# Kernel optimization log

Hardware: AMD Instinct MI355X
Metric: run time of the kernel (lower is better)

## Reference

```python
import jax, jax.numpy as jnp
import numpy as np

B, C, H, W = 8, 256, 64, 64
IC = 64  # inter_channels


def conv1x1(x, w, b):
    # x: [B,C,H,W], w: [O,C], b: [O]
    return jnp.einsum('bchw,oc->bohw', x, w) + b[None, :, None, None]


def maxpool2(x):
    # 2x2 max pool, stride 2. x: [B,C,H,W]
    b, c, h, w = x.shape
    return x.reshape(b, c, h // 2, 2, w // 2, 2).max(axis=(3, 5))


def setup_inputs() -> dict:
    key = jax.random.key(0)
    ks = jax.random.split(key, 9)
    s_in = 1.0 / np.sqrt(C)
    s_ic = 1.0 / np.sqrt(IC)
    return {
        'x': jax.random.normal(ks[0], (B, C, H, W), dtype=jnp.float32),
        'g_w': jax.random.uniform(ks[1], (IC, C), jnp.float32, -s_in, s_in),
        'g_b': jax.random.uniform(ks[2], (IC,), jnp.float32, -s_in, s_in),
        'theta_w': jax.random.uniform(ks[3], (IC, C), jnp.float32, -s_in, s_in),
        'theta_b': jax.random.uniform(ks[4], (IC,), jnp.float32, -s_in, s_in),
        'phi_w': jax.random.uniform(ks[5], (IC, C), jnp.float32, -s_in, s_in),
        'phi_b': jax.random.uniform(ks[6], (IC,), jnp.float32, -s_in, s_in),
        'W_w': jax.random.uniform(ks[7], (C, IC), jnp.float32, -np.sqrt(6.0 / IC), np.sqrt(6.0 / IC)),
        'W_b': jax.random.uniform(ks[8], (C,), jnp.float32, -s_ic, s_ic),
    }


def reference(x, g_w, g_b, theta_w, theta_b, phi_w, phi_b, W_w, W_b):
    b, c, h, w = x.shape
    n = h * w                     # query positions
    m = (h // 2) * (w // 2)       # pooled key/value positions

    v = maxpool2(conv1x1(x, g_w, g_b)).reshape(b, IC, m).transpose(0, 2, 1)   # [b,m,ic]
    q = conv1x1(x, theta_w, theta_b).reshape(b, IC, n).transpose(0, 2, 1)     # [b,n,ic]
    k = maxpool2(conv1x1(x, phi_w, phi_b)).reshape(b, IC, m)                  # [b,ic,m]

    attn = jax.nn.softmax(jnp.einsum('bni,bim->bnm', q, k), axis=-1)          # [b,n,m]
    attended = jnp.einsum('bnm,bmi->bni', attn, v)                            # [b,n,ic]
    attended = attended.transpose(0, 2, 1).reshape(b, IC, h, w)
    # F.interpolate to (h,w) is identity here: attended already has spatial (h,w)
    return conv1x1(attended, W_w, W_b) + x
```

## Files before the change

kernel.cpp:

```cpp
#include <hip/hip_runtime.h>

typedef unsigned short ushort_t;
typedef unsigned int   uint_t;

typedef __attribute__((ext_vector_type(8))) short  short8;
typedef __attribute__((ext_vector_type(4))) short  short4v;
typedef __attribute__((ext_vector_type(4))) float  float4v;

#define BB    8
#define CC    256
#define HH    64
#define WW2   64
#define NPIX  4096
#define MPOS  1024
#define ICH   64

__device__ __forceinline__ float bf2f(ushort_t u) {
  return __uint_as_float(((uint_t)u) << 16);
}
__device__ __forceinline__ ushort_t f2bf(float f) {
  uint_t i = __float_as_uint(f);
  uint_t r = (i + 0x7FFFu + ((i >> 16) & 1u)) >> 16;
  return (ushort_t)r;
}
__device__ __forceinline__ ushort_t f2bf_rna(float f) {
  return (ushort_t)((__float_as_uint(f) + 0x8000u) >> 16);
}
__device__ __forceinline__ uint_t pack2(float a, float b) {
  return (uint_t)f2bf(a) | ((uint_t)f2bf(b) << 16);
}

__global__ __launch_bounds__(256) void prep_kernel(
    const float* __restrict__ theta_w, const float* __restrict__ phi_w,
    const float* __restrict__ g_w, const float* __restrict__ W_w,
    const float* __restrict__ theta_b, const float* __restrict__ phi_b,
    const float* __restrict__ g_b,
    ushort_t* __restrict__ wA2, ushort_t* __restrict__ Wbf2,
    float* __restrict__ biasAll) {
  int i = blockIdx.x * 256 + threadIdx.x;
  if (i < 49152) {
    float v = (i < 16384) ? theta_w[i]
            : (i < 32768) ? phi_w[i - 16384]
                          : g_w[i - 32768];
    int o = i >> 8, c = i & 255;
    wA2[(c >> 3) * 1536 + o * 8 + (c & 7)] = f2bf(v);
  } else if (i < 65536) {
    int j = i - 49152;
    int o = j >> 6, ic = j & 63;
    Wbf2[(ic >> 3) * 2048 + o * 8 + (ic & 7)] = f2bf(W_w[j]);
  } else if (i < 65600)    biasAll[i - 65536] = theta_b[i - 65536];
  else if (i < 65664)      biasAll[i - 65536] = phi_b[i - 65600];
  else if (i < 65728)      biasAll[i - 65536] = g_b[i - 65664];
}

__global__ __launch_bounds__(256, 2) void qkv_kernel(
    const float* __restrict__ x, const ushort_t* __restrict__ wA2,
    const float* __restrict__ biasAll,
    ushort_t* __restrict__ qbuf, ushort_t* __restrict__ kTbuf,
    ushort_t* __restrict__ vTbuf) {
  __shared__ __align__(16) ushort_t Bsu[64 * 256];
  uint4* Bs16 = (uint4*)Bsu;
  int tid = threadIdx.x;
  int wave = tid >> 6, lane = tid & 63;
  int quad = lane >> 4, col = lane & 15;
  int b = blockIdx.x >> 6, t = blockIdx.x & 63;
  int rj = t >> 1, h = t & 1;

  {
    int pos = tid & 63, cg = tid >> 6;
    int prow = pos >> 5, pcol = pos & 31;
    const float* xsrc = x + (size_t)b * (CC * NPIX) +
                        (size_t)(2 * rj + prow) * WW2 + h * 32 + pcol;
#pragma unroll
    for (int g = 0; g < 8; ++g) {
      float v[8];
#pragma unroll
      for (int j = 0; j < 8; ++j)
        v[j] = xsrc[(size_t)(cg * 64 + g * 8 + j) * NPIX];
      uint4 w;
      w.x = pack2(v[0], v[1]);
      w.y = pack2(v[2], v[3]);
      w.z = pack2(v[4], v[5]);
      w.w = pack2(v[6], v[7]);
      int jb = cg * 8 + g;
      Bs16[pos * 32 + (jb & ~7) + ((jb & 7) ^ (pos & 7))] = w;
    }
  }
  __syncthreads();

  float4v acc[3][4];
#pragma unroll
  for (int ot = 0; ot < 3; ++ot) {
    int ob = wave * 48 + ot * 16 + quad * 4;
    float4v bv;
#pragma unroll
    for (int r = 0; r < 4; ++r) bv[r] = biasAll[ob + r];
#pragma unroll
    for (int s = 0; s < 4; ++s) acc[ot][s] = bv;
  }

  const uint4* wA16 = (const uint4*)wA2;
#pragma unroll
  for (int ks = 0; ks < 8; ++ks) {
    int kblk = ks * 4 + quad;
    short8 aw[3];
#pragma unroll
    for (int ot = 0; ot < 3; ++ot) {
      uint4 a = wA16[kblk * 192 + wave * 48 + ot * 16 + col];
      aw[ot] = *(const short8*)&a;
    }
#pragma unroll
    for (int s = 0; s < 4; ++s) {
      int lp = s * 16 + col;
      uint4 braw = Bs16[lp * 32 + (kblk & ~7) + ((kblk & 7) ^ (lp & 7))];
      short8 bx = *(const short8*)&braw;
#pragma unroll
      for (int ot = 0; ot < 3; ++ot)
        acc[ot][s] = __builtin_amdgcn_mfma_f32_16x16x32_bf16(aw[ot], bx, acc[ot][s], 0, 0, 0);
    }
  }

#pragma unroll
  for (int ot = 0; ot < 3; ++ot) {
    int ob = wave * 48 + ot * 16;
    if (ob < 64) {
#pragma unroll
      for (int s = 0; s < 4; ++s) {
        int n = (2 * rj + (s >> 1)) * WW2 + h * 32 + (s & 1) * 16 + col;
        uint2 u;
        u.x = pack2(acc[ot][s][0], acc[ot][s][1]);
        u.y = pack2(acc[ot][s][2], acc[ot][s][3]);
        *(uint2*)&qbuf[((size_t)(b * NPIX + n)) * ICH + ob + quad * 4] = u;
      }
    } else if (ob < 128) {
#pragma unroll
      for (int s = 0; s < 2; ++s) {
        float4v pm;
#pragma unroll
        for (int r = 0; r < 4; ++r) {
          float v = fmaxf(acc[ot][s][r], acc[ot][s + 2][r]);
          pm[r] = fmaxf(v, __shfl_xor(v, 1));
        }
        if ((lane & 1) == 0) {
          int m = rj * 32 + h * 16 + s * 8 + (col >> 1);
          uint2 u;
          u.x = pack2(pm[0], pm[1]);
          u.y = pack2(pm[2], pm[3]);
          *(uint2*)&kTbuf[((size_t)(b * MPOS + m)) * ICH + (ob - 64) + quad * 4] = u;
        }
      }
    } else {
#pragma unroll
      for (int s = 0; s < 2; ++s) {
        float4v pm;
#pragma unroll
        for (int r = 0; r < 4; ++r) {
          float v = fmaxf(acc[ot][s][r], acc[ot][s + 2][r]);
          pm[r] = fmaxf(v, __shfl_xor(v, 1));
        }
        if ((lane & 1) == 0) {
          int m = rj * 32 + h * 16 + s * 8 + (col >> 1);
#pragma unroll
          for (int r = 0; r < 4; ++r)
            vTbuf[((size_t)(b * ICH + (ob - 128) + quad * 4 + r)) * MPOS + m] = f2bf(pm[r]);
        }
      }
    }
  }
}

__global__ __launch_bounds__(256, 2) void attn_out_kernel(
    const ushort_t* __restrict__ qbuf, const ushort_t* __restrict__ kTbuf,
    const ushort_t* __restrict__ vTbuf, const ushort_t* __restrict__ Wbf2,
    const float* __restrict__ W_b, const float* __restrict__ x,
    float* __restrict__ out) {
  __shared__ __align__(16) ushort_t Ks[2][64 * 64];
  __shared__ __align__(16) ushort_t Vs[2][64 * 64];
  __shared__ __align__(16) ushort_t Ps[64 * 72];
  int tid  = threadIdx.x;
  int wave = tid >> 6, lane = tid & 63;
  int quad = lane >> 4, col = lane & 15;
  int b = blockIdx.x >> 6, qt = blockIdx.x & 63;

  const ushort_t* qrow = qbuf + ((size_t)(b * NPIX + qt * 64 + wave * 16 + col)) * ICH;
  short8 aQ0 = *(const short8*)&qrow[quad * 8];
  short8 aQ1 = *(const short8*)&qrow[32 + quad * 8];

  int krow0 = tid >> 3,           kblk0 = tid & 7;
  int krow1 = (tid + 256) >> 3,   kblk1 = tid & 7;
  int vic = tid >> 2, vseg = tid & 3;

  const uint4* ksrc0 = (const uint4*)(kTbuf + ((size_t)(b * MPOS)) * ICH);
  const ushort_t* vbase = vTbuf + ((size_t)(b * ICH + vic)) * MPOS;

  {
    uint4 k0 = ksrc0[tid], k1 = ksrc0[tid + 256];
    const uint4* vsrc = (const uint4*)(vbase + vseg * 16);
    uint4 v0 = vsrc[0], v1 = vsrc[1];
    *(uint4*)&Ks[0][krow0 * 64 + ((kblk0 ^ (krow0 & 7)) * 8)] = k0;
    *(uint4*)&Ks[0][krow1 * 64 + ((kblk1 ^ (krow1 & 7)) * 8)] = k1;
    *(uint4*)&Vs[0][vic * 64 + (((vseg * 2 + 0) ^ (vic & 7)) * 8)] = v0;
    *(uint4*)&Vs[0][vic * 64 + (((vseg * 2 + 1) ^ (vic & 7)) * 8)] = v1;
  }
  __syncthreads();

  const float4v zero4 = {0.f, 0.f, 0.f, 0.f};
  float l_lane[4] = {0.f, 0.f, 0.f, 0.f};
  float4v o_acc[4];
#pragma unroll
  for (int t = 0; t < 4; ++t) o_acc[t] = zero4;

  for (int kt = 0; kt < 16; ++kt) {
    uint4 nk0, nk1, nv0, nv1;
    if (kt < 15) {
      const uint4* ksrc = (const uint4*)(kTbuf + ((size_t)(b * MPOS + (kt + 1) * 64)) * ICH);
      nk0 = ksrc[tid];
      nk1 = ksrc[tid + 256];
      const uint4* vsrc = (const uint4*)(vbase + (kt + 1) * 64 + vseg * 16);
      nv0 = vsrc[0];
      nv1 = vsrc[1];
    }
    int buf = kt & 1;

    float4v s_acc[4];
#pragma unroll
    for (int t = 0; t < 4; ++t) {
      float4v s = zero4;
      short8 bk0 = *(const short8*)&Ks[buf][(t * 16 + col) * 64 + ((quad ^ (col & 7)) * 8)];
      s = __builtin_amdgcn_mfma_f32_16x16x32_bf16(aQ0, bk0, s, 0, 0, 0);
      short8 bk1 = *(const short8*)&Ks[buf][(t * 16 + col) * 64 + (((4 + quad) ^ (col & 7)) * 8)];
      s = __builtin_amdgcn_mfma_f32_16x16x32_bf16(aQ1, bk1, s, 0, 0, 0);
      s_acc[t] = s;
    }

#pragma unroll
    for (int r = 0; r < 4; ++r) {
      int prow = (wave * 16 + quad * 4 + r) * 72;
#pragma unroll
      for (int t = 0; t < 4; ++t) {
        float pv = __expf(s_acc[t][r]);
        l_lane[r] += pv;
        Ps[prow + t * 16 + col] = f2bf_rna(pv);
      }
    }

#pragma unroll
    for (int kk = 0; kk < 2; ++kk) {
      short8 ap = *(const short8*)&Ps[(wave * 16 + col) * 72 + kk * 32 + quad * 8];
#pragma unroll
      for (int t = 0; t < 4; ++t) {
        short8 bv = *(const short8*)&Vs[buf][(t * 16 + col) * 64 + (((kk * 4 + quad) ^ (col & 7)) * 8)];
        o_acc[t] = __builtin_amdgcn_mfma_f32_16x16x32_bf16(ap, bv, o_acc[t], 0, 0, 0);
      }
    }

    if (kt < 15) {
      int nbuf = buf ^ 1;
      *(uint4*)&Ks[nbuf][krow0 * 64 + ((kblk0 ^ (krow0 & 7)) * 8)] = nk0;
      *(uint4*)&Ks[nbuf][krow1 * 64 + ((kblk1 ^ (krow1 & 7)) * 8)] = nk1;
      *(uint4*)&Vs[nbuf][vic * 64 + (((vseg * 2 + 0) ^ (vic & 7)) * 8)] = nv0;
      *(uint4*)&Vs[nbuf][vic * 64 + (((vseg * 2 + 1) ^ (vic & 7)) * 8)] = nv1;
      __syncthreads();
    }
  }

#pragma unroll
  for (int r = 0; r < 4; ++r) {
    float l = l_lane[r];
    l += __shfl_xor(l, 1);
    l += __shfl_xor(l, 2);
    l += __shfl_xor(l, 4);
    l += __shfl_xor(l, 8);
    float inv = 1.0f / l;
    int prow = (wave * 16 + quad * 4 + r) * 72;
#pragma unroll
    for (int t = 0; t < 4; ++t)
      Ps[prow + t * 16 + col] = f2bf(o_acc[t][r] * inv);
  }

  float4v cacc[16];
#pragma unroll
  for (int ot = 0; ot < 16; ++ot) {
    float bv = W_b[ot * 16 + col];
    float4v bvec = {bv, bv, bv, bv};
    cacc[ot] = bvec;
  }
  const uint4* W16 = (const uint4*)Wbf2;
#pragma unroll
  for (int ks = 0; ks < 2; ++ks) {
    short8 ap = *(const short8*)&Ps[(wave * 16 + col) * 72 + ks * 32 + quad * 8];
#pragma unroll
    for (int ot = 0; ot < 16; ++ot) {
      uint4 wr = W16[(ks * 4 + quad) * 256 + ot * 16 + col];
      short8 wf = *(const short8*)&wr;
      cacc[ot] = __builtin_amdgcn_mfma_f32_16x16x32_bf16(ap, wf, cacc[ot], 0, 0, 0);
    }
  }

  int pbase = qt * 64 + wave * 16 + quad * 4;
#pragma unroll
  for (int ot = 0; ot < 16; ++ot) {
    int o = ot * 16 + col;
    size_t idx = ((size_t)(b * CC + o)) * NPIX + pbase;
    float4 xv = *(const float4*)&x[idx];
    float4 ov;
    ov.x = cacc[ot][0] + xv.x;
    ov.y = cacc[ot][1] + xv.y;
    ov.z = cacc[ot][2] + xv.z;
    ov.w = cacc[ot][3] + xv.w;
    *(float4*)&out[idx] = ov;
  }
}

extern "C" void kernel_launch(void* const* d_in, const int* in_sizes, int n_in,
                              void* d_out, int out_size, void* d_ws, size_t ws_size,
                              hipStream_t stream) {
  const float* x       = (const float*)d_in[0];
  const float* g_w     = (const float*)d_in[1];
  const float* g_b     = (const float*)d_in[2];
  const float* theta_w = (const float*)d_in[3];
  const float* theta_b = (const float*)d_in[4];
  const float* phi_w   = (const float*)d_in[5];
  const float* phi_b   = (const float*)d_in[6];
  const float* W_w     = (const float*)d_in[7];
  const float* W_b     = (const float*)d_in[8];
  (void)in_sizes; (void)n_in; (void)out_size; (void)ws_size;

  char* ws = (char*)d_ws;
  ushort_t* wA2     = (ushort_t*)(ws + 0);
  ushort_t* Wbf2    = (ushort_t*)(ws + 98304);
  float*    biasAll = (float*)(ws + 131072);
  ushort_t* qbuf    = (ushort_t*)(ws + 262144);
  ushort_t* kTbuf   = (ushort_t*)(ws + 4456448);
  ushort_t* vTbuf   = (ushort_t*)(ws + 5505024);
  float* out = (float*)d_out;

  prep_kernel<<<257, 256, 0, stream>>>(theta_w, phi_w, g_w, W_w,
                                       theta_b, phi_b, g_b,
                                       wA2, Wbf2, biasAll);
  qkv_kernel<<<512, 256, 0, stream>>>(x, wA2, biasAll, qbuf, kTbuf, vTbuf);
  attn_out_kernel<<<512, 256, 0, stream>>>(qbuf, kTbuf, vTbuf, Wbf2, W_b, x, out);
}
```

Baseline: 132.2 us.

## Load K/V MFMA fragments directly from global memory instead of LDS staging

```diff
diff --git a/kernel.cpp b/kernel.cpp
--- a/kernel.cpp
+++ b/kernel.cpp
@@ -169,13 +169,11 @@
   }
 }
 
-__global__ __launch_bounds__(256, 2) void attn_out_kernel(
+__global__ __launch_bounds__(256, 4) void attn_out_kernel(
     const ushort_t* __restrict__ qbuf, const ushort_t* __restrict__ kTbuf,
     const ushort_t* __restrict__ vTbuf, const ushort_t* __restrict__ Wbf2,
     const float* __restrict__ W_b, const float* __restrict__ x,
     float* __restrict__ out) {
-  __shared__ __align__(16) ushort_t Ks[2][64 * 64];
-  __shared__ __align__(16) ushort_t Vs[2][64 * 64];
   __shared__ __align__(16) ushort_t Ps[64 * 72];
   int tid  = threadIdx.x;
   int wave = tid >> 6, lane = tid & 63;
@@ -186,23 +184,8 @@
   short8 aQ0 = *(const short8*)&qrow[quad * 8];
   short8 aQ1 = *(const short8*)&qrow[32 + quad * 8];
 
-  int krow0 = tid >> 3,           kblk0 = tid & 7;
-  int krow1 = (tid + 256) >> 3,   kblk1 = tid & 7;
-  int vic = tid >> 2, vseg = tid & 3;
-
-  const uint4* ksrc0 = (const uint4*)(kTbuf + ((size_t)(b * MPOS)) * ICH);
-  const ushort_t* vbase = vTbuf + ((size_t)(b * ICH + vic)) * MPOS;
-
-  {
-    uint4 k0 = ksrc0[tid], k1 = ksrc0[tid + 256];
-    const uint4* vsrc = (const uint4*)(vbase + vseg * 16);
-    uint4 v0 = vsrc[0], v1 = vsrc[1];
-    *(uint4*)&Ks[0][krow0 * 64 + ((kblk0 ^ (krow0 & 7)) * 8)] = k0;
-    *(uint4*)&Ks[0][krow1 * 64 + ((kblk1 ^ (krow1 & 7)) * 8)] = k1;
-    *(uint4*)&Vs[0][vic * 64 + (((vseg * 2 + 0) ^ (vic & 7)) * 8)] = v0;
-    *(uint4*)&Vs[0][vic * 64 + (((vseg * 2 + 1) ^ (vic & 7)) * 8)] = v1;
-  }
-  __syncthreads();
+  const ushort_t* kfrag = kTbuf + ((size_t)(b * MPOS + col)) * ICH + quad * 8;
+  const ushort_t* vfrag = vTbuf + ((size_t)(b * ICH + col)) * MPOS + quad * 8;
 
   const float4v zero4 = {0.f, 0.f, 0.f, 0.f};
   float l_lane[4] = {0.f, 0.f, 0.f, 0.f};
@@ -211,24 +194,14 @@
   for (int t = 0; t < 4; ++t) o_acc[t] = zero4;
 
   for (int kt = 0; kt < 16; ++kt) {
-    uint4 nk0, nk1, nv0, nv1;
-    if (kt < 15) {
-      const uint4* ksrc = (const uint4*)(kTbuf + ((size_t)(b * MPOS + (kt + 1) * 64)) * ICH);
-      nk0 = ksrc[tid];
-      nk1 = ksrc[tid + 256];
-      const uint4* vsrc = (const uint4*)(vbase + (kt + 1) * 64 + vseg * 16);
-      nv0 = vsrc[0];
-      nv1 = vsrc[1];
-    }
-    int buf = kt & 1;
-
     float4v s_acc[4];
 #pragma unroll
     for (int t = 0; t < 4; ++t) {
+      const ushort_t* kr = kfrag + (size_t)(kt * 64 + t * 16) * ICH;
       float4v s = zero4;
-      short8 bk0 = *(const short8*)&Ks[buf][(t * 16 + col) * 64 + ((quad ^ (col & 7)) * 8)];
+      short8 bk0 = *(const short8*)&kr[0];
       s = __builtin_amdgcn_mfma_f32_16x16x32_bf16(aQ0, bk0, s, 0, 0, 0);
-      short8 bk1 = *(const short8*)&Ks[buf][(t * 16 + col) * 64 + (((4 + quad) ^ (col & 7)) * 8)];
+      short8 bk1 = *(const short8*)&kr[32];
       s = __builtin_amdgcn_mfma_f32_16x16x32_bf16(aQ1, bk1, s, 0, 0, 0);
       s_acc[t] = s;
     }
@@ -249,18 +222,10 @@
       short8 ap = *(const short8*)&Ps[(wave * 16 + col) * 72 + kk * 32 + quad * 8];
 #pragma unroll
       for (int t = 0; t < 4; ++t) {
-        short8 bv = *(const short8*)&Vs[buf][(t * 16 + col) * 64 + (((kk * 4 + quad) ^ (col & 7)) * 8)];
+        const ushort_t* vr = vfrag + (size_t)(t * 16) * MPOS + kt * 64 + kk * 32;
+        short8 bv = *(const short8*)&vr[0];
         o_acc[t] = __builtin_amdgcn_mfma_f32_16x16x32_bf16(ap, bv, o_acc[t], 0, 0, 0);
       }
-    }
-
-    if (kt < 15) {
-      int nbuf = buf ^ 1;
-      *(uint4*)&Ks[nbuf][krow0 * 64 + ((kblk0 ^ (krow0 & 7)) * 8)] = nk0;
-      *(uint4*)&Ks[nbuf][krow1 * 64 + ((kblk1 ^ (krow1 & 7)) * 8)] = nk1;
-      *(uint4*)&Vs[nbuf][vic * 64 + (((vseg * 2 + 0) ^ (vic & 7)) * 8)] = nv0;
-      *(uint4*)&Vs[nbuf][vic * 64 + (((vseg * 2 + 1) ^ (vic & 7)) * 8)] = nv1;
-      __syncthreads();
     }
   }
 
```

Result: slower. 171.4 us (+29.6%).
